# Performance work log

Hardware: AMD Instinct MI355X
Metric: run time of the kernel (lower is better)

Reference implementation:

```python
import jax, jax.numpy as jnp
import numpy as np

DS_DIM = 2
N_EXPERTS = 64
N_CLASSES = 26
IMG = 68
BATCH = 8192
FLAT = 1960  # 10 * 14 * 14 after two conv+pool stages


def _conv2d(x, w, b):
    # x: [B, Cin, H, W], w: [Cout, Cin, kh, kw]
    y = jax.lax.conv_general_dilated(
        x, w, window_strides=(1, 1), padding='VALID',
        dimension_numbers=('NCHW', 'OIHW', 'NCHW'))
    return y + b[None, :, None, None]


def _maxpool2(x):
    return jax.lax.reduce_window(
        x, -jnp.inf, jax.lax.max,
        window_dimensions=(1, 1, 2, 2), window_strides=(1, 1, 2, 2),
        padding='VALID')


def setup_inputs() -> dict:
    key = jax.random.key(0)
    ks = jax.random.split(key, 14)
    x = jax.random.normal(ks[0], (BATCH, DS_DIM), dtype=jnp.float32)
    cls_idx = jax.random.randint(ks[1], (BATCH,), 0, N_CLASSES)
    images = jax.random.normal(ks[2], (N_CLASSES, 1, IMG, IMG), dtype=jnp.float32)
    s = 0.05
    conv1_w = jax.random.normal(ks[3], (5, 1, 5, 5), dtype=jnp.float32) * s
    conv1_b = jax.random.normal(ks[4], (5,), dtype=jnp.float32) * s
    conv2_w = jax.random.normal(ks[5], (10, 5, 5, 5), dtype=jnp.float32) * s
    conv2_b = jax.random.normal(ks[6], (10,), dtype=jnp.float32) * s
    fc1_w = jax.random.normal(ks[7], (500, FLAT + DS_DIM), dtype=jnp.float32) * s
    fc1_b = jax.random.normal(ks[8], (500,), dtype=jnp.float32) * s
    fc2_w = jax.random.normal(ks[9], (N_EXPERTS, 500), dtype=jnp.float32) * s
    fc2_b = jax.random.normal(ks[10], (N_EXPERTS,), dtype=jnp.float32) * s
    # geotorch-constrained expert matrices: B_A positive-semidefinite, C_A skew
    raw_b = jax.random.normal(ks[11], (N_EXPERTS, DS_DIM, DS_DIM), dtype=jnp.float32)
    A_B = jnp.einsum('nik,njk->nij', raw_b, raw_b) * 0.1        # PSD
    raw_c = jax.random.normal(ks[12], (N_EXPERTS, DS_DIM, DS_DIM), dtype=jnp.float32)
    A_C = (raw_c - jnp.swapaxes(raw_c, -1, -2)) * 0.5            # skew
    x_tar = jax.random.normal(ks[13], (1, DS_DIM), dtype=jnp.float32)
    return {'x': x, 'cls_idx': cls_idx, 'images': images,
            'conv1_w': conv1_w, 'conv1_b': conv1_b,
            'conv2_w': conv2_w, 'conv2_b': conv2_b,
            'fc1_w': fc1_w, 'fc1_b': fc1_b,
            'fc2_w': fc2_w, 'fc2_b': fc2_b,
            'A_B': A_B, 'A_C': A_C, 'x_tar': x_tar}


def reference(x, cls_idx, images, conv1_w, conv1_b, conv2_w, conv2_b,
              fc1_w, fc1_b, fc2_w, fc2_b, A_B, A_C, x_tar):
    # gating CNN: gather per-sample image by class index
    img = images[cls_idx]                             # [B, 1, 68, 68]
    h = _maxpool2(jax.nn.relu(_conv2d(img, conv1_w, conv1_b)))   # [B, 5, 32, 32]
    h = _maxpool2(jax.nn.relu(_conv2d(h, conv2_w, conv2_b)))     # [B, 10, 14, 14]
    h = h.reshape(h.shape[0], -1)                     # [B, 1960]
    h = jnp.concatenate([h, x], axis=1)               # [B, 1962]
    h = jax.nn.relu(h @ fc1_w.T + fc1_b)              # [B, 500]
    w_all = jax.nn.softmax(h @ fc2_w.T + fc2_b, axis=1)  # [B, N]
    # fused expert weighted-sum (original: python loop over N tiny matmuls)
    A = A_B + A_C                                     # [N, d, d]
    diff = x_tar - x                                  # [B, d]
    s_all = jnp.einsum('bn,nij,bj->bi', w_all, A, diff)
    return s_all
```

## Files before the change

kernel.cpp:

```cpp
#include <hip/hip_runtime.h>

#define WS_FEAT   0
#define WS_FC1P   50960
#define WS_W2     63960
#define WS_AFLAT  95960
#define WS_WX     96216

__global__ __launch_bounds__(256) void k_cnn(
    const float* __restrict__ images,
    const float* __restrict__ c1w, const float* __restrict__ c1b,
    const float* __restrict__ c2w, const float* __restrict__ c2b,
    const float* __restrict__ fc2w, const float* __restrict__ fc1w,
    const float* __restrict__ A_B, const float* __restrict__ A_C,
    float* __restrict__ ws)
{
    const int b = blockIdx.x, t = threadIdx.x;
    if (b >= 260) {
        if (b == 260) {
            float* W2 = ws + WS_W2;
            for (int i = t; i < 32000; i += 256) {
                int k = i >> 6, e = i & 63;
                W2[i] = fc2w[e * 500 + k];
            }
        } else {
            float* Af = ws + WS_AFLAT;
            if (t < 256) Af[t] = A_B[t] + A_C[t];
            float* Wx = ws + WS_WX;
            for (int i = t; i < 1000; i += 256) {
                int j = i >> 1, k = i & 1;
                Wx[i] = fc1w[j * 1962 + 1960 + k];
            }
        }
        return;
    }

    const int c = b / 10, oc = b - c * 10;

    __shared__ float simg[4624];
    __shared__ float sc1[5 * 32 * 34];
    __shared__ float sw1[125];
    __shared__ float sb1[5];
    __shared__ float sw2[125];

    {
        const float* im = images + c * 4624;
        for (int i = t; i < 2312; i += 256)
            *(float2*)&simg[2 * i] = *(const float2*)&im[2 * i];
        for (int i = t; i < 125; i += 256) sw1[i] = c1w[i];
        if (t < 5) sb1[t] = c1b[t];
        for (int i = t; i < 125; i += 256) sw2[i] = c2w[oc * 125 + i];
    }
    __syncthreads();

#pragma unroll
    for (int r = 0; r < 4; ++r) {
        const int pos = t + 256 * r;
        const int py = pos >> 5, px = pos & 31;
        float ir[6][6];
#pragma unroll
        for (int a = 0; a < 6; ++a)
#pragma unroll
            for (int q = 0; q < 3; ++q) {
                float2 v = *(const float2*)&simg[(2 * py + a) * 68 + 2 * px + 2 * q];
                ir[a][2 * q] = v.x; ir[a][2 * q + 1] = v.y;
            }
#pragma unroll
        for (int o = 0; o < 5; ++o) {
            float bias = sb1[o];
            float a00 = bias, a01 = bias, a10 = bias, a11 = bias;
#pragma unroll
            for (int ky = 0; ky < 5; ++ky)
#pragma unroll
                for (int kx = 0; kx < 5; ++kx) {
                    float w = sw1[o * 25 + ky * 5 + kx];
                    a00 += w * ir[ky][kx];     a01 += w * ir[ky][kx + 1];
                    a10 += w * ir[ky + 1][kx]; a11 += w * ir[ky + 1][kx + 1];
                }
            sc1[o * 1088 + py * 34 + px] =
                fmaxf(fmaxf(fmaxf(a00, a01), fmaxf(a10, a11)), 0.f);
        }
    }
    __syncthreads();

    if (t < 196) {
        const int py = t / 14, px = t - py * 14;
        const float bias = c2b[oc];
        float a00 = bias, a01 = bias, a10 = bias, a11 = bias;
#pragma unroll
        for (int ic = 0; ic < 5; ++ic) {
            float ir[6][6];
#pragma unroll
            for (int a = 0; a < 6; ++a)
#pragma unroll
                for (int q = 0; q < 3; ++q) {
                    float2 v = *(const float2*)&sc1[ic * 1088 + (2 * py + a) * 34 + 2 * px + 2 * q];
                    ir[a][2 * q] = v.x; ir[a][2 * q + 1] = v.y;
                }
#pragma unroll
            for (int ky = 0; ky < 5; ++ky)
#pragma unroll
                for (int kx = 0; kx < 5; ++kx) {
                    float w = sw2[ic * 25 + ky * 5 + kx];
                    a00 += w * ir[ky][kx];     a01 += w * ir[ky][kx + 1];
                    a10 += w * ir[ky + 1][kx]; a11 += w * ir[ky + 1][kx + 1];
                }
        }
        float v = fmaxf(fmaxf(fmaxf(a00, a01), fmaxf(a10, a11)), 0.f);
        ws[WS_FEAT + c * 1960 + oc * 196 + py * 14 + px] = v;
    }
}

__global__ __launch_bounds__(256) void k_fc1(
    const float* __restrict__ fc1w, const float* __restrict__ fc1b,
    float* __restrict__ ws)
{
    const int lane = threadIdx.x & 63, w = threadIdx.x >> 6;
    const int c = blockIdx.x / 63, jg = blockIdx.x - c * 63;
    const int j0 = jg * 8 + 2 * w;
    if (j0 >= 500) return;
    const int j1 = j0 + 1;

    const float* f  = ws + WS_FEAT + c * 1960;
    const float* w0 = fc1w + j0 * 1962;
    const float* w1 = fc1w + j1 * 1962;

    float acc0 = 0.f, acc1 = 0.f;
#pragma unroll
    for (int i = 0; i < 30; ++i) {
        int k = lane + 64 * i;
        float fv = f[k];
        acc0 += w0[k] * fv;
        acc1 += w1[k] * fv;
    }
    {
        int k = lane + 1920;
        if (k < 1960) {
            float fv = f[k];
            acc0 += w0[k] * fv;
            acc1 += w1[k] * fv;
        }
    }
#pragma unroll
    for (int off = 32; off >= 1; off >>= 1) {
        acc0 += __shfl_xor(acc0, off);
        acc1 += __shfl_xor(acc1, off);
    }
    if (lane == 0) {
        ws[WS_FC1P + c * 500 + j0] = acc0 + fc1b[j0];
        ws[WS_FC1P + c * 500 + j1] = acc1 + fc1b[j1];
    }
}

__global__ __launch_bounds__(256) void k_moe(
    const float* __restrict__ x, const int* __restrict__ cls,
    const float* __restrict__ fc2b, const float* __restrict__ x_tar,
    const float* __restrict__ ws, float* __restrict__ out)
{
    __shared__ float hs[16 * 508];
    __shared__ float lg[4 * 16 * 64];
    const int t = threadIdx.x;
    const int b0 = blockIdx.x * 16;
    const float* fc1p = ws + WS_FC1P;
    const float* Wx   = ws + WS_WX;
    const float* W2   = ws + WS_W2;
    const float* Af   = ws + WS_AFLAT;

    {
        const int sl = t >> 4;
        const int j0 = t & 15;
        const int b  = b0 + sl;
        const int c  = cls[b];
        const float x0 = x[2 * b], x1 = x[2 * b + 1];
        const float* fr = fc1p + c * 500;
        float* hr = hs + sl * 508;
        for (int j = j0; j < 500; j += 16) {
            float2 wx = *(const float2*)&Wx[2 * j];
            hr[j] = fmaxf(fr[j] + x0 * wx.x + x1 * wx.y, 0.f);
        }
    }
    __syncthreads();

    {
        const int kq = __builtin_amdgcn_readfirstlane(t >> 6);
        const int rr = t & 63;
        const int e0 = (rr >> 2) * 4;
        const int s0 = (rr & 3) * 4;
        const int kbeg = kq * 128;
        const int kcnt = (kq == 3) ? 116 : 128;

        float4 a0 = make_float4(0.f, 0.f, 0.f, 0.f);
        float4 a1 = a0, a2 = a0, a3 = a0;
        const float* h0p = hs + (s0 + 0) * 508;
        const float* h1p = hs + (s0 + 1) * 508;
        const float* h2p = hs + (s0 + 2) * 508;
        const float* h3p = hs + (s0 + 3) * 508;

        for (int k = kbeg; k < kbeg + kcnt; k += 4) {
            float4 w0 = *(const float4*)&W2[(k + 0) * 64 + e0];
            float4 w1 = *(const float4*)&W2[(k + 1) * 64 + e0];
            float4 w2 = *(const float4*)&W2[(k + 2) * 64 + e0];
            float4 w3 = *(const float4*)&W2[(k + 3) * 64 + e0];
            float4 h0 = *(const float4*)&h0p[k];
            float4 h1 = *(const float4*)&h1p[k];
            float4 h2 = *(const float4*)&h2p[k];
            float4 h3 = *(const float4*)&h3p[k];
            a0.x += h0.x*w0.x + h0.y*w1.x + h0.z*w2.x + h0.w*w3.x;
            a0.y += h0.x*w0.y + h0.y*w1.y + h0.z*w2.y + h0.w*w3.y;
            a0.z += h0.x*w0.z + h0.y*w1.z + h0.z*w2.z + h0.w*w3.z;
            a0.w += h0.x*w0.w + h0.y*w1.w + h0.z*w2.w + h0.w*w3.w;
            a1.x += h1.x*w0.x + h1.y*w1.x + h1.z*w2.x + h1.w*w3.x;
            a1.y += h1.x*w0.y + h1.y*w1.y + h1.z*w2.y + h1.w*w3.y;
            a1.z += h1.x*w0.z + h1.y*w1.z + h1.z*w2.z + h1.w*w3.z;
            a1.w += h1.x*w0.w + h1.y*w1.w + h1.z*w2.w + h1.w*w3.w;
            a2.x += h2.x*w0.x + h2.y*w1.x + h2.z*w2.x + h2.w*w3.x;
            a2.y += h2.x*w0.y + h2.y*w1.y + h2.z*w2.y + h2.w*w3.y;
            a2.z += h2.x*w0.z + h2.y*w1.z + h2.z*w2.z + h2.w*w3.z;
            a2.w += h2.x*w0.w + h2.y*w1.w + h2.z*w2.w + h2.w*w3.w;
            a3.x += h3.x*w0.x + h3.y*w1.x + h3.z*w2.x + h3.w*w3.x;
            a3.y += h3.x*w0.y + h3.y*w1.y + h3.z*w2.y + h3.w*w3.y;
            a3.z += h3.x*w0.z + h3.y*w1.z + h3.z*w2.z + h3.w*w3.z;
            a3.w += h3.x*w0.w + h3.y*w1.w + h3.z*w2.w + h3.w*w3.w;
        }
        *(float4*)&lg[(kq * 16 + s0 + 0) * 64 + e0] = a0;
        *(float4*)&lg[(kq * 16 + s0 + 1) * 64 + e0] = a1;
        *(float4*)&lg[(kq * 16 + s0 + 2) * 64 + e0] = a2;
        *(float4*)&lg[(kq * 16 + s0 + 3) * 64 + e0] = a3;
    }
    __syncthreads();

    {
        const int wv_ = t >> 6;
        const int e   = t & 63;
        const float xt0 = x_tar[0], xt1 = x_tar[1];
        const float be = fc2b[e];
        const float4 a4 = *(const float4*)&Af[4 * e];
#pragma unroll
        for (int i = 0; i < 4; ++i) {
            const int s = wv_ * 4 + i;
            float logit = be + lg[s * 64 + e] + lg[(16 + s) * 64 + e]
                        + lg[(32 + s) * 64 + e] + lg[(48 + s) * 64 + e];
            float m = logit;
#pragma unroll
            for (int off = 32; off >= 1; off >>= 1) m = fmaxf(m, __shfl_xor(m, off));
            float ex = __expf(logit - m);
            float sum = ex;
            float m0 = ex * a4.x, m1 = ex * a4.y, m2 = ex * a4.z, m3 = ex * a4.w;
#pragma unroll
            for (int off = 32; off >= 1; off >>= 1) {
                sum += __shfl_xor(sum, off);
                m0 += __shfl_xor(m0, off);
                m1 += __shfl_xor(m1, off);
                m2 += __shfl_xor(m2, off);
                m3 += __shfl_xor(m3, off);
            }
            if (e == 0) {
                const int b = b0 + s;
                float d0 = xt0 - x[2 * b], d1 = xt1 - x[2 * b + 1];
                float inv = 1.f / sum;
                out[2 * b]     = (m0 * d0 + m1 * d1) * inv;
                out[2 * b + 1] = (m2 * d0 + m3 * d1) * inv;
            }
        }
    }
}

extern "C" void kernel_launch(void* const* d_in, const int* in_sizes, int n_in,
                              void* d_out, int out_size, void* d_ws, size_t ws_size,
                              hipStream_t stream) {
    const float* x      = (const float*)d_in[0];
    const int*   cls    = (const int*)  d_in[1];
    const float* images = (const float*)d_in[2];
    const float* c1w    = (const float*)d_in[3];
    const float* c1b    = (const float*)d_in[4];
    const float* c2w    = (const float*)d_in[5];
    const float* c2b    = (const float*)d_in[6];
    const float* fc1w   = (const float*)d_in[7];
    const float* fc1b   = (const float*)d_in[8];
    const float* fc2w   = (const float*)d_in[9];
    const float* fc2b   = (const float*)d_in[10];
    const float* A_B    = (const float*)d_in[11];
    const float* A_C    = (const float*)d_in[12];
    const float* x_tar  = (const float*)d_in[13];
    float* out = (float*)d_out;
    float* ws  = (float*)d_ws;

    k_cnn<<<262, 256, 0, stream>>>(images, c1w, c1b, c2w, c2b, fc2w, fc1w,
                                   A_B, A_C, ws);
    k_fc1<<<1638, 256, 0, stream>>>(fc1w, fc1b, ws);
    k_moe<<<512, 256, 0, stream>>>(x, cls, fc2b, x_tar, ws, out);
}
```

Baseline: 145.4 us.

## Split CNN gating conv into spatial quadrant blocks with per-channel partial sums

Each (class, output channel) block is split into four spatial quadrants, launching 1040 CNN blocks instead of 260. Each block loads only its 40x40 image tile and computes an 18x18 conv1 halo region. Conv2 work is also spread across input channels using 245 threads, with a shared-memory reduction at the end. The aim is to fill more compute units and use more threads in conv2. The cost is redundant conv1 work on halo overlap and an extra barrier.

Result: faster. 142.1 us (-2.3%).

```diff
diff --git a/kernel.cpp b/kernel.cpp
--- a/kernel.cpp
+++ b/kernel.cpp
@@ -15,8 +15,8 @@
     float* __restrict__ ws)
 {
     const int b = blockIdx.x, t = threadIdx.x;
-    if (b >= 260) {
-        if (b == 260) {
+    if (b >= 1040) {
+        if (b == 1040) {
             float* W2 = ws + WS_W2;
             for (int i = t; i < 32000; i += 256) {
                 int k = i >> 6, e = i & 63;
@@ -34,35 +34,37 @@
         return;
     }
 
-    const int c = b / 10, oc = b - c * 10;
-
-    __shared__ float simg[4624];
-    __shared__ float sc1[5 * 32 * 34];
+    const int c  = b / 40, r = b - c * 40;
+    const int oc = r >> 2, q = r & 3;
+    const int qy = q >> 1, qx = q & 1;
+
+    __shared__ float simg[1600];
+    __shared__ float sc1[1620];
     __shared__ float sw1[125];
     __shared__ float sb1[5];
     __shared__ float sw2[125];
-
-    {
-        const float* im = images + c * 4624;
-        for (int i = t; i < 2312; i += 256)
-            *(float2*)&simg[2 * i] = *(const float2*)&im[2 * i];
-        for (int i = t; i < 125; i += 256) sw1[i] = c1w[i];
+    __shared__ float part[980];
+
+    {
+        const float* ib = images + c * 4624 + (28 * qy) * 68 + 28 * qx;
+        for (int i = t; i < 800; i += 256) {
+            int row = i / 20, col = i - row * 20;
+            *(float2*)&simg[row * 40 + 2 * col] = *(const float2*)&ib[row * 68 + 2 * col];
+        }
+        if (t < 125) { sw1[t] = c1w[t]; sw2[t] = c2w[oc * 125 + t]; }
         if (t < 5) sb1[t] = c1b[t];
-        for (int i = t; i < 125; i += 256) sw2[i] = c2w[oc * 125 + i];
-    }
-    __syncthreads();
-
-#pragma unroll
-    for (int r = 0; r < 4; ++r) {
-        const int pos = t + 256 * r;
-        const int py = pos >> 5, px = pos & 31;
+    }
+    __syncthreads();
+
+    for (int idx = t; idx < 324; idx += 256) {
+        int ry = idx / 18, rx = idx - ry * 18;
         float ir[6][6];
 #pragma unroll
         for (int a = 0; a < 6; ++a)
 #pragma unroll
-            for (int q = 0; q < 3; ++q) {
-                float2 v = *(const float2*)&simg[(2 * py + a) * 68 + 2 * px + 2 * q];
-                ir[a][2 * q] = v.x; ir[a][2 * q + 1] = v.y;
+            for (int q2 = 0; q2 < 3; ++q2) {
+                float2 v = *(const float2*)&simg[(2 * ry + a) * 40 + 2 * rx + 2 * q2];
+                ir[a][2 * q2] = v.x; ir[a][2 * q2 + 1] = v.y;
             }
 #pragma unroll
         for (int o = 0; o < 5; ++o) {
@@ -76,37 +78,50 @@
                     a00 += w * ir[ky][kx];     a01 += w * ir[ky][kx + 1];
                     a10 += w * ir[ky + 1][kx]; a11 += w * ir[ky + 1][kx + 1];
                 }
-            sc1[o * 1088 + py * 34 + px] =
+            sc1[o * 324 + idx] =
                 fmaxf(fmaxf(fmaxf(a00, a01), fmaxf(a10, a11)), 0.f);
         }
     }
     __syncthreads();
 
-    if (t < 196) {
-        const int py = t / 14, px = t - py * 14;
+    if (t < 245) {
+        const int ic = t / 49, pos = t - ic * 49;
+        const int py = pos / 7, px = pos - py * 7;
+        float ir[6][6];
+#pragma unroll
+        for (int a = 0; a < 6; ++a)
+#pragma unroll
+            for (int q2 = 0; q2 < 3; ++q2) {
+                float2 v = *(const float2*)&sc1[ic * 324 + (2 * py + a) * 18 + 2 * px + 2 * q2];
+                ir[a][2 * q2] = v.x; ir[a][2 * q2 + 1] = v.y;
+            }
+        float p00 = 0.f, p01 = 0.f, p10 = 0.f, p11 = 0.f;
+#pragma unroll
+        for (int ky = 0; ky < 5; ++ky)
+#pragma unroll
+            for (int kx = 0; kx < 5; ++kx) {
+                float w = sw2[ic * 25 + ky * 5 + kx];
+                p00 += w * ir[ky][kx];     p01 += w * ir[ky][kx + 1];
+                p10 += w * ir[ky + 1][kx]; p11 += w * ir[ky + 1][kx + 1];
+            }
+        part[(pos * 4 + 0) * 5 + ic] = p00;
+        part[(pos * 4 + 1) * 5 + ic] = p01;
+        part[(pos * 4 + 2) * 5 + ic] = p10;
+        part[(pos * 4 + 3) * 5 + ic] = p11;
+    }
+    __syncthreads();
+
+    if (t < 49) {
+        const int py = t / 7, px = t - py * 7;
         const float bias = c2b[oc];
-        float a00 = bias, a01 = bias, a10 = bias, a11 = bias;
-#pragma unroll
-        for (int ic = 0; ic < 5; ++ic) {
-            float ir[6][6];
-#pragma unroll
-            for (int a = 0; a < 6; ++a)
-#pragma unroll
-                for (int q = 0; q < 3; ++q) {
-                    float2 v = *(const float2*)&sc1[ic * 1088 + (2 * py + a) * 34 + 2 * px + 2 * q];
-                    ir[a][2 * q] = v.x; ir[a][2 * q + 1] = v.y;
-                }
-#pragma unroll
-            for (int ky = 0; ky < 5; ++ky)
-#pragma unroll
-                for (int kx = 0; kx < 5; ++kx) {
-                    float w = sw2[ic * 25 + ky * 5 + kx];
-                    a00 += w * ir[ky][kx];     a01 += w * ir[ky][kx + 1];
-                    a10 += w * ir[ky + 1][kx]; a11 += w * ir[ky + 1][kx + 1];
-                }
-        }
-        float v = fmaxf(fmaxf(fmaxf(a00, a01), fmaxf(a10, a11)), 0.f);
-        ws[WS_FEAT + c * 1960 + oc * 196 + py * 14 + px] = v;
+        const float* pp = part + t * 20;
+        float s0 = ((((pp[0]  + pp[1])  + pp[2])  + pp[3])  + pp[4])  + bias;
+        float s1 = ((((pp[5]  + pp[6])  + pp[7])  + pp[8])  + pp[9])  + bias;
+        float s2 = ((((pp[10] + pp[11]) + pp[12]) + pp[13]) + pp[14]) + bias;
+        float s3 = ((((pp[15] + pp[16]) + pp[17]) + pp[18]) + pp[19]) + bias;
+        float v = fmaxf(fmaxf(fmaxf(s0, s1), fmaxf(s2, s3)), 0.f);
+        const int gpy = qy * 7 + py, gpx = qx * 7 + px;
+        ws[WS_FEAT + c * 1960 + oc * 196 + gpy * 14 + gpx] = v;
     }
 }
 
@@ -284,8 +299,8 @@
     float* out = (float*)d_out;
     float* ws  = (float*)d_ws;
 
-    k_cnn<<<262, 256, 0, stream>>>(images, c1w, c1b, c2w, c2b, fc2w, fc1w,
-                                   A_B, A_C, ws);
+    k_cnn<<<1042, 256, 0, stream>>>(images, c1w, c1b, c2w, c2b, fc2w, fc1w,
+                                    A_B, A_C, ws);
     k_fc1<<<1638, 256, 0, stream>>>(fc1w, fc1b, ws);
     k_moe<<<512, 256, 0, stream>>>(x, cls, fc2b, x_tar, ws, out);
 }
```
